# Kernel optimization log

Hardware: AMD Instinct MI355X
Metric: run time of the kernel (lower is better)

Reference implementation:

```python
import jax, jax.numpy as jnp
import numpy as np

B, A, DIN, HID, HEADS, NOUT, K = 256, 64, 64, 128, 4, 2, 7
N = B * A                      # 16384 nodes
C = HID                        # per-head dim == out_channels (module quirk)
SCALE = (HID // HEADS) ** -0.5 # 1/sqrt(32), as in the module


def _xavier(k, shape):
    fan_out, fan_in = shape
    lim = (6.0 / (fan_in + fan_out)) ** 0.5
    return jax.random.uniform(k, shape, jnp.float32, -lim, lim)


def setup_inputs() -> dict:
    key = jax.random.key(0)
    ks = jax.random.split(key, 24)
    x = jax.random.normal(ks[0], (N, DIN), jnp.float32)
    pos_b = jax.random.uniform(ks[1], (B, A, 2), jnp.float32) * 10.0  # [B,A,2]
    pos = pos_b.reshape(N, 2)

    # kNN graph per environment (replicates torch.cdist + topk smallest, drop self)
    d = jnp.linalg.norm(pos_b[:, :, None, :] - pos_b[:, None, :, :], axis=-1)  # [B,A,A]
    _, idx = jax.lax.top_k(-d, K + 1)
    nb = idx[..., 1:]                                   # [B,A,K] neighbor ids
    offs = (jnp.arange(B) * A)[:, None, None]
    src = jnp.broadcast_to(jnp.arange(A)[None, :, None], (B, A, K)) + offs
    dst = nb + offs
    loops = jnp.arange(N)
    edge_index = jnp.stack([
        jnp.concatenate([src.reshape(-1), loops]),
        jnp.concatenate([dst.reshape(-1), loops]),
    ]).astype(jnp.int32)                                # [2, E], E = B*A*K + N

    inp = {"x": x, "pos": pos, "edge_index": edge_index}
    inp["l0_Wq"] = _xavier(ks[2], (HEADS * C, 2))
    inp["l0_Wk"] = _xavier(ks[3], (HEADS * C, 2))
    inp["l0_Wv"] = _xavier(ks[4], (HEADS * C, DIN))
    inp["l0_Wo"] = _xavier(ks[5], (HID, HEADS * C))
    inp["l0_bo"] = jnp.zeros((HID,), jnp.float32)
    inp["l1_Wq"] = _xavier(ks[6], (HEADS * C, 2))
    inp["l1_Wk"] = _xavier(ks[7], (HEADS * C, 2))
    inp["l1_Wv"] = _xavier(ks[8], (HEADS * C, HID))
    inp["l1_Wo"] = _xavier(ks[9], (HID, HEADS * C))
    inp["l1_bo"] = jnp.zeros((HID,), jnp.float32)
    inp["W1"] = _xavier(ks[10], (256, HID))
    inp["b1"] = jnp.zeros((256,), jnp.float32)
    inp["W2"] = _xavier(ks[11], (256, 256))
    inp["b2"] = jnp.zeros((256,), jnp.float32)
    inp["W3"] = _xavier(ks[12], (NOUT, 256))
    inp["b3"] = jnp.zeros((NOUT,), jnp.float32)
    return inp


def _gat(x, pos, src, dst, Wq, Wk, Wv, Wo, bo):
    # positions -> Q/K, features -> V (position-aware attention)
    q = (pos @ Wq.T).reshape(N, HEADS, C)
    k = (pos @ Wk.T).reshape(N, HEADS, C)
    v = (x @ Wv.T).reshape(N, HEADS, C)
    # per-edge logits, segment softmax over incoming edges of dst
    alpha = jnp.einsum('ehc,ehc->eh', q[dst], k[src]) * SCALE        # [E,H]
    amax = jax.ops.segment_max(alpha, dst, num_segments=N)           # [N,H]
    ex = jnp.exp(alpha - amax[dst])
    a = ex / jax.ops.segment_sum(ex, dst, num_segments=N)[dst]
    msg = v[src] * a[..., None]                                      # [E,H,C]
    agg = jax.ops.segment_sum(msg, dst, num_segments=N)              # [N,H,C]
    return agg.reshape(N, HEADS * C) @ Wo.T + bo


def reference(x, pos, edge_index,
              l0_Wq, l0_Wk, l0_Wv, l0_Wo, l0_bo,
              l1_Wq, l1_Wk, l1_Wv, l1_Wo, l1_bo,
              W1, b1, W2, b2, W3, b3):
    src, dst = edge_index[0], edge_index[1]
    h = jnp.tanh(_gat(x, pos, src, dst, l0_Wq, l0_Wk, l0_Wv, l0_Wo, l0_bo))
    h = jnp.tanh(_gat(h, pos, src, dst, l1_Wq, l1_Wk, l1_Wv, l1_Wo, l1_bo))
    h = jax.nn.relu(h @ W1.T + b1)
    h = jax.nn.relu(h @ W2.T + b2)
    out = h @ W3.T + b3
    return out.reshape(B, A, NOUT)
```

## Files before the change

### kernel.cpp

```cpp
#include <hip/hip_runtime.h>
#include <hip/hip_bf16.h>
#include <cstddef>
#include <math.h>

#define N_NODES 16384
#define DIN 64
#define HID 128
#define SCALE_F 0.17677669529663687f

using bf16x8 = __attribute__((ext_vector_type(8))) short;
using f32x4  = __attribute__((ext_vector_type(4))) float;

__device__ __forceinline__ ushort f2b(float x) {
  __hip_bfloat16 h = __float2bfloat16(x);
  return *(ushort*)&h;
}
__device__ __forceinline__ float b2f(ushort u) {
  __hip_bfloat16 h = *(__hip_bfloat16*)&u;
  return __bfloat162float(h);
}
__device__ __forceinline__ void split1(float x, ushort& h, ushort& l) {
  h = f2b(x);
  l = f2b(x - b2f(h));
}
__device__ __forceinline__ void split3(float x, ushort& a, ushort& b, ushort& c) {
  a = f2b(x);
  float r1 = x - b2f(a);
  b = f2b(r1);
  c = f2b(r1 - b2f(b));
}

#define MFMA(d, A, B) d = __builtin_amdgcn_mfma_f32_16x16x32_bf16(A, B, d, 0, 0, 0)


__global__ __launch_bounds__(256) void prep_all_kernel(
    const float* __restrict__ Wq0, const float* __restrict__ Wk0,
    const float* __restrict__ Wq1, const float* __restrict__ Wk1,
    float* __restrict__ G,
    const float* __restrict__ Wv0, const float* __restrict__ Wo0,
    ushort* __restrict__ M0a, ushort* __restrict__ M0b, ushort* __restrict__ M0c,
    const float* __restrict__ Wv1, const float* __restrict__ Wo1,
    ushort* __restrict__ M1a, ushort* __restrict__ M1b, ushort* __restrict__ M1c,
    const float* __restrict__ W1, ushort* __restrict__ W1hi, ushort* __restrict__ W1lo,
    const float* __restrict__ W2, ushort* __restrict__ W2hi, ushort* __restrict__ W2lo,
    unsigned long long* __restrict__ out64)
{
  int blk = blockIdx.x, t = threadIdx.x;
  if (blk == 0) {
    if (t >= 32) return;
    int l = t >> 4, h = (t >> 2) & 3, a = (t >> 1) & 1, b = t & 1;
    const float* Wq = l ? Wq1 : Wq0;
    const float* Wk = l ? Wk1 : Wk0;
    float acc = 0.f;
    for (int c = 0; c < 128; c++)
      acc += Wq[(h * 128 + c) * 2 + a] * Wk[(h * 128 + c) * 2 + b];
    G[t] = acc;
  } else if (blk < 97) {
    int D, gidx;
    const float *Wv, *Wo;
    ushort *Ma, *Mb, *Mc;
    if (blk < 33) { D = DIN; gidx = (blk - 1) * 256 + t;  Wv = Wv0; Wo = Wo0; Ma = M0a; Mb = M0b; Mc = M0c; }
    else          { D = HID; gidx = (blk - 33) * 256 + t; Wv = Wv1; Wo = Wo1; Ma = M1a; Mb = M1b; Mc = M1c; }
    int o = gidx / D, rem = gidx - o * D;
    int qD = D >> 2;
    int h = rem / qD, d0 = (rem - h * qD) * 4;
    const float* wv = Wv + (size_t)(h * 128) * D + d0;
    const float* wo = Wo + (size_t)o * 512 + h * 128;
    float ax = 0.f, ay = 0.f, az = 0.f, aw = 0.f;
    for (int c = 0; c < 128; c++) {
      float4 v = *(const float4*)&wv[(size_t)c * D];
      float w = wo[c];
      ax += v.x * w; ay += v.y * w; az += v.z * w; aw += v.w * w;
    }
    int idx = o * (4 * D) + h * D + d0;
    ushort4 ua, ub, uc;
    split3(ax, ua.x, ub.x, uc.x);
    split3(ay, ua.y, ub.y, uc.y);
    split3(az, ua.z, ub.z, uc.z);
    split3(aw, ua.w, ub.w, uc.w);
    *(ushort4*)&Ma[idx] = ua;
    *(ushort4*)&Mb[idx] = ub;
    *(ushort4*)&Mc[idx] = uc;
  } else if (blk < 193) {
    if (blk < 129) {
      int i = ((blk - 97) * 256 + t) * 4;
      float4 w = *(const float4*)&W1[i];
      ushort4 hi, lo;
      split1(w.x, hi.x, lo.x); split1(w.y, hi.y, lo.y);
      split1(w.z, hi.z, lo.z); split1(w.w, hi.w, lo.w);
      *(ushort4*)&W1hi[i] = hi;
      *(ushort4*)&W1lo[i] = lo;
    } else {
      int j = ((blk - 129) * 256 + t) * 4;
      float4 w = *(const float4*)&W2[j];
      ushort4 hi, lo;
      split1(w.x, hi.x, lo.x); split1(w.y, hi.y, lo.y);
      split1(w.z, hi.z, lo.z); split1(w.w, hi.w, lo.w);
      *(ushort4*)&W2hi[j] = hi;
      *(ushort4*)&W2lo[j] = lo;
    }
  } else {
    int i = (blk - 193) * 256 + t;
    ((float4*)out64)[i] = (float4){0.f, 0.f, 0.f, 0.f};
  }
}


#define SFB_OFF 8192
#define SFC_OFF 16384
#define PXS_OFF 24576
#define PYS_OFF 24704
#define SMASK_OFF 24832
#define AFRAG_OFF 25088
#define PH_OFF 57856
#define LDS_USHORTS 74752

template <int KD>
__device__ __forceinline__ void gat_layer(
    int wave, int lane, int lm, int lq,
    const ushort* sFa, const ushort* sFb, const ushort* sFc,
    ushort* aA,
    const float* pxs, const float* pys,
    const unsigned long long* smask,
    const float* __restrict__ G,
    const ushort* __restrict__ Ma, const ushort* __restrict__ Mb,
    const ushort* __restrict__ Mc,
    f32x4 hacc[4])
{
  constexpr int NKF = KD / 32;
  const int K4 = 4 * KD;
  const int o = 16 * (wave & 7) + lm;
  const int hb = wave >> 3;

  bf16x8 nA, nB, nC;
  {
    size_t boff = (size_t)o * K4 + (2 * hb) * KD + lq * 8;
    nA = *(const bf16x8*)&Ma[boff];
    nB = *(const bf16x8*)&Mb[boff];
    nC = *(const bf16x8*)&Mc[boff];
  }

  {
    int wm = wave & 3;
    int h = wave >> 2;
    float pdxm = pxs[wm * 16 + lm];
    float pdym = pys[wm * 16 + lm];
    unsigned long long mm = smask[wm * 16 + lm];
    unsigned mb0 = (unsigned)((mm >> (8 * lq)) & 0xFF);
    unsigned mb1 = (unsigned)((mm >> (32 + 8 * lq)) & 0xFF);
    float g0 = G[h * 4], g1 = G[h * 4 + 1], g2 = G[h * 4 + 2], g3 = G[h * 4 + 3];
    float a0 = (g0 * pdxm + g2 * pdym) * SCALE_F;
    float a1 = (g1 * pdxm + g3 * pdym) * SCALE_F;
    float sshift = a0 * pdxm + a1 * pdym;
    float e[16];
    float sum = 0.f;
#pragma unroll
    for (int j = 0; j < 8; j++) {
      e[j]     = ((mb0 >> j) & 1) ? __expf(a0 * pxs[8 * lq + j] + a1 * pys[8 * lq + j] - sshift) : 0.f;
      e[8 + j] = ((mb1 >> j) & 1) ? __expf(a0 * pxs[32 + 8 * lq + j] + a1 * pys[32 + 8 * lq + j] - sshift) : 0.f;
      sum += e[j] + e[8 + j];
    }
    sum += __shfl_xor(sum, 16);
    sum += __shfl_xor(sum, 32);
    float inv = 1.f / sum;
    bf16x8 Aa0, Aa1, Ab0, Ab1;
#pragma unroll
    for (int j = 0; j < 8; j++) {
      ushort ua, ub;
      split1(e[j] * inv, ua, ub);     Aa0[j] = (short)ua; Ab0[j] = (short)ub;
      split1(e[8 + j] * inv, ua, ub); Aa1[j] = (short)ua; Ab1[j] = (short)ub;
    }
    int sbase = wave * 2048 + lane * 8;
    *(bf16x8*)&aA[sbase]        = Aa0;
    *(bf16x8*)&aA[sbase + 512]  = Aa1;
    *(bf16x8*)&aA[sbase + 1024] = Ab0;
    *(bf16x8*)&aA[sbase + 1536] = Ab1;
  }
  __syncthreads();

#pragma unroll
  for (int i = 0; i < 4; i++) hacc[i] = (f32x4){0.f, 0.f, 0.f, 0.f};

#pragma unroll 1
  for (int hi = 0; hi < 2; hi++) {
    int h = 2 * hb + hi;
    f32x4 y[4];
#pragma unroll
    for (int i = 0; i < 4; i++) y[i] = (f32x4){0.f, 0.f, 0.f, 0.f};
#pragma unroll 1
    for (int kf = 0; kf < NKF; kf++) {
      int ko = kf * 32 + lq * 8;
      int sw = lm << 3;
      bf16x8 ma = nA, mb = nB, mc = nC;
#pragma unroll
      for (int mp = 0; mp < 2; mp++) {
        int f0 = (mp * 32 + lm) * 128 + (ko ^ sw);
        int f1 = f0 + 16 * 128;
        bf16x8 fa0 = *(const bf16x8*)&sFa[f0], fa1 = *(const bf16x8*)&sFa[f1];
        bf16x8 fb0 = *(const bf16x8*)&sFb[f0], fb1 = *(const bf16x8*)&sFb[f1];
        bf16x8 fc0 = *(const bf16x8*)&sFc[f0], fc1 = *(const bf16x8*)&sFc[f1];
        f32x4 y0 = y[mp * 2], y1 = y[mp * 2 + 1];
        MFMA(y0, fa0, ma); MFMA(y1, fa1, ma);
        MFMA(y0, fa0, mb); MFMA(y1, fa1, mb);
        MFMA(y0, fb0, ma); MFMA(y1, fb1, ma);
        MFMA(y0, fa0, mc); MFMA(y1, fa1, mc);
        MFMA(y0, fc0, ma); MFMA(y1, fc1, ma);
        MFMA(y0, fb0, mb); MFMA(y1, fb1, mb);
        y[mp * 2] = y0; y[mp * 2 + 1] = y1;
      }
      if (hi == 0 || kf != NKF - 1) {
        int hn = (kf == NKF - 1) ? (h + 1) : h;
        int kn = (kf == NKF - 1) ? 0 : (kf + 1);
        size_t boff = (size_t)o * K4 + hn * KD + kn * 32 + lq * 8;
        nA = *(const bf16x8*)&Ma[boff];
        nB = *(const bf16x8*)&Mb[boff];
        nC = *(const bf16x8*)&Mc[boff];
      }
    }
    bf16x8 Ya[2], Yb[2];
#pragma unroll
    for (int kb = 0; kb < 2; kb++) {
#pragma unroll
      for (int j = 0; j < 8; j++) {
        int sl = ((2 * lq + (j >> 2)) & 3) * 16 + lm;
        float v0 = __shfl(y[2 * kb][j & 3], sl);
        float v1 = __shfl(y[2 * kb + 1][j & 3], sl);
        float v = (lq & 2) ? v1 : v0;
        ushort ua, ub;
        split1(v, ua, ub);
        Ya[kb][j] = (short)ua; Yb[kb][j] = (short)ub;
      }
    }
#pragma unroll
    for (int mtd = 0; mtd < 4; mtd++) {
      int abase = (h * 4 + mtd) * 2048 + lane * 8;
      bf16x8 Aa0 = *(const bf16x8*)&aA[abase];
      bf16x8 Aa1 = *(const bf16x8*)&aA[abase + 512];
      bf16x8 Ab0 = *(const bf16x8*)&aA[abase + 1024];
      bf16x8 Ab1 = *(const bf16x8*)&aA[abase + 1536];
      MFMA(hacc[mtd], Aa0, Ya[0]);
      MFMA(hacc[mtd], Aa0, Yb[0]);
      MFMA(hacc[mtd], Ab0, Ya[0]);
      MFMA(hacc[mtd], Ab0, Yb[0]);
      MFMA(hacc[mtd], Aa1, Ya[1]);
      MFMA(hacc[mtd], Aa1, Yb[1]);
      MFMA(hacc[mtd], Ab1, Ya[1]);
      MFMA(hacc[mtd], Ab1, Yb[1]);
    }
  }
}

__global__ __attribute__((amdgpu_flat_work_group_size(1024, 1024), amdgpu_waves_per_eu(4, 4)))
void fused_gat_kernel(
    const float* __restrict__ x, const float* __restrict__ pos,
    const int* __restrict__ srcp, const int* __restrict__ dstp,
    const float* __restrict__ G,
    const ushort* __restrict__ M0a, const ushort* __restrict__ M0b, const ushort* __restrict__ M0c,
    const ushort* __restrict__ M1a, const ushort* __restrict__ M1b, const ushort* __restrict__ M1c,
    const float* __restrict__ bo0, const float* __restrict__ bo1,
    const ushort* __restrict__ W1hi, const ushort* __restrict__ W1lo, const float* __restrict__ b1,
    const ushort* __restrict__ W2hi, const ushort* __restrict__ W2lo, const float* __restrict__ b2,
    const float* __restrict__ W3, const float* __restrict__ b3,
    float* __restrict__ outp)
{
  __shared__ __align__(16) ushort uBig[LDS_USHORTS];
  ushort* sFa = uBig;
  ushort* sFb = uBig + SFB_OFF;
  ushort* sFc = uBig + SFC_OFF;
  float* pxs = (float*)(uBig + PXS_OFF);
  float* pys = (float*)(uBig + PYS_OFF);
  unsigned long long* smask = (unsigned long long*)(uBig + SMASK_OFF);
  ushort* aA = uBig + AFRAG_OFF;
  ushort* pA = uBig + AFRAG_OFF;
  ushort* pB = uBig + AFRAG_OFF + 16384;
  float* pH = (float*)(uBig + PH_OFF);

  int b = blockIdx.x, t = threadIdx.x;
  int wave = t >> 6, lane = t & 63, lm = lane & 15, lq = lane >> 4;
  int o = 16 * (wave & 7) + lm;

  int e_s = 0, e_d = 0;
  if (t < 448) {
    e_s = srcp[b * 448 + t];
    e_d = dstp[b * 448 + t];
  }
  float posx = 0.f, posy = 0.f;
  if (t < 64) {
    posx = pos[(b * 64 + t) * 2];
    posy = pos[(b * 64 + t) * 2 + 1];
  }
  const float4* gx = (const float4*)(x + (size_t)b * 64 * DIN);
  float4 xv = gx[t];
  float bv0 = bo0[o];
  float bv1 = bo1[o];

  if (t < 64) {
    pxs[t] = posx;
    pys[t] = posy;
    smask[t] = 1ull << t;
  }
  {
    int r = t >> 4, c = (t & 15) * 4;
    int cs = c ^ ((r & 15) << 3);
    ushort4 ua, ub, uc;
    split3(xv.x, ua.x, ub.x, uc.x); split3(xv.y, ua.y, ub.y, uc.y);
    split3(xv.z, ua.z, ub.z, uc.z); split3(xv.w, ua.w, ub.w, uc.w);
    *(ushort4*)&sFa[r * 128 + cs] = ua;
    *(ushort4*)&sFb[r * 128 + cs] = ub;
    *(ushort4*)&sFc[r * 128 + cs] = uc;
  }
  __syncthreads();
  if (t < 448) {
    atomicOr(&smask[e_d & 63], 1ull << (e_s & 63));
  }
  __syncthreads();

  f32x4 hacc[4];
  gat_layer<DIN>(wave, lane, lm, lq, sFa, sFb, sFc, aA, pxs, pys, smask,
                 G, M0a, M0b, M0c, hacc);
  if (wave >= 8) {
#pragma unroll
    for (int mtd = 0; mtd < 4; mtd++)
#pragma unroll
      for (int r = 0; r < 4; r++)
        pH[(mtd * 16 + lq * 4 + r) * 132 + o] = hacc[mtd][r];
  }
  __syncthreads();
  if (wave < 8) {
#pragma unroll
    for (int mtd = 0; mtd < 4; mtd++)
#pragma unroll
      for (int r = 0; r < 4; r++) {
        int dst = mtd * 16 + lq * 4 + r;
        float v = tanhf(hacc[mtd][r] + pH[dst * 132 + o] + bv0);
        ushort ua, ub, uc;
        split3(v, ua, ub, uc);
        int cs = o ^ ((dst & 15) << 3);
        sFa[dst * 128 + cs] = ua;
        sFb[dst * 128 + cs] = ub;
        sFc[dst * 128 + cs] = uc;
      }
  }
  __syncthreads();
  gat_layer<HID>(wave, lane, lm, lq, sFa, sFb, sFc, aA, pxs, pys, smask,
                 G + 16, M1a, M1b, M1c, hacc);

  int col = 16 * wave + lm;
  bf16x8 pw1h[4], pw1l[4];
#pragma unroll
  for (int kf = 0; kf < 4; kf++) {
    int ko = kf * 32 + lq * 8;
    pw1h[kf] = *(const bf16x8*)&W1hi[(size_t)col * 128 + ko];
    pw1l[kf] = *(const bf16x8*)&W1lo[(size_t)col * 128 + ko];
  }
  float b1v = b1[col];

  if (wave >= 8) {
#pragma unroll
    for (int mtd = 0; mtd < 4; mtd++)
#pragma unroll
      for (int r = 0; r < 4; r++)
        pH[(mtd * 16 + lq * 4 + r) * 132 + o] = hacc[mtd][r];
  }
  __syncthreads();
  if (wave < 8) {
#pragma unroll
    for (int mtd = 0; mtd < 4; mtd++)
#pragma unroll
      for (int r = 0; r < 4; r++) {
        int dst = mtd * 16 + lq * 4 + r;
        float v = tanhf(hacc[mtd][r] + pH[dst * 132 + o] + bv1);
        ushort hh, ll;
        split1(v, hh, ll);
        int cs = o ^ ((dst & 15) << 3);
        sFa[dst * 128 + cs] = hh;
        sFb[dst * 128 + cs] = ll;
      }
  }
  __syncthreads();
  f32x4 y1[4];
#pragma unroll
  for (int mtd = 0; mtd < 4; mtd++) y1[mtd] = (f32x4){0.f, 0.f, 0.f, 0.f};
#pragma unroll
  for (int kf = 0; kf < 4; kf++) {
    int ko = kf * 32 + lq * 8;
    bf16x8 bh = pw1h[kf];
    bf16x8 bl = pw1l[kf];
#pragma unroll
    for (int mtd = 0; mtd < 4; mtd++) {
      int row = mtd * 16 + lm;
      int cs = ko ^ (lm << 3);
      bf16x8 ah = *(const bf16x8*)&sFa[row * 128 + cs];
      bf16x8 al = *(const bf16x8*)&sFb[row * 128 + cs];
      MFMA(y1[mtd], ah, bh);
      MFMA(y1[mtd], ah, bl);
      MFMA(y1[mtd], al, bh);
    }
  }
  {
#pragma unroll
    for (int mtd = 0; mtd < 4; mtd++)
#pragma unroll
      for (int r = 0; r < 4; r++) {
        int row = mtd * 16 + lq * 4 + r;
        float v = fmaxf(y1[mtd][r] + b1v, 0.f);
        ushort hh, ll;
        split1(v, hh, ll);
        int cc = col ^ ((row & 15) << 3);
        pA[row * 256 + cc] = hh;
        pB[row * 256 + cc] = ll;
      }
  }
  bf16x8 pw2h[8], pw2l[8];
#pragma unroll
  for (int kf = 0; kf < 8; kf++) {
    int ko = kf * 32 + lq * 8;
    pw2h[kf] = *(const bf16x8*)&W2hi[(size_t)col * 256 + ko];
    pw2l[kf] = *(const bf16x8*)&W2lo[(size_t)col * 256 + ko];
  }
  float w30 = W3[col], w31 = W3[256 + col];
  float b20 = b2[col];
  float bb0 = (wave == 0) ? b3[0] : 0.f;
  float bb1 = (wave == 0) ? b3[1] : 0.f;
  __syncthreads();
  f32x4 y2[4];
#pragma unroll
  for (int mtd = 0; mtd < 4; mtd++) y2[mtd] = (f32x4){0.f, 0.f, 0.f, 0.f};
#pragma unroll
  for (int kf = 0; kf < 8; kf++) {
    int ko = kf * 32 + lq * 8;
    bf16x8 bh = pw2h[kf];
    bf16x8 bl = pw2l[kf];
#pragma unroll
    for (int mtd = 0; mtd < 4; mtd++) {
      int row = mtd * 16 + lm;
      int cc = ko ^ (lm << 3);
      bf16x8 ah = *(const bf16x8*)&pA[row * 256 + cc];
      bf16x8 al = *(const bf16x8*)&pB[row * 256 + cc];
      MFMA(y2[mtd], ah, bh);
      MFMA(y2[mtd], ah, bl);
      MFMA(y2[mtd], al, bh);
    }
  }
  {
#pragma unroll
    for (int mtd = 0; mtd < 4; mtd++)
#pragma unroll
      for (int r = 0; r < 4; r++) {
        float va = fmaxf(y2[mtd][r] + b20, 0.f);
        float s0 = va * w30;
        float s1 = va * w31;
        s0 += __shfl_xor(s0, 1); s0 += __shfl_xor(s0, 2);
        s0 += __shfl_xor(s0, 4); s0 += __shfl_xor(s0, 8);
        s1 += __shfl_xor(s1, 1); s1 += __shfl_xor(s1, 2);
        s1 += __shfl_xor(s1, 4); s1 += __shfl_xor(s1, 8);
        if (lm == 0) {
          int row = b * 64 + mtd * 16 + lq * 4 + r;
          atomicAdd(&outp[row * 2 + 0], s0 + bb0);
          atomicAdd(&outp[row * 2 + 1], s1 + bb1);
        }
      }
  }
}


extern "C" void kernel_launch(void* const* d_in, const int* in_sizes, int n_in,
                              void* d_out, int out_size, void* d_ws, size_t ws_size,
                              hipStream_t stream) {
  const float* x     = (const float*)d_in[0];
  const float* pos   = (const float*)d_in[1];
  const int*   ei    = (const int*)d_in[2];
  const float* l0_Wq = (const float*)d_in[3];
  const float* l0_Wk = (const float*)d_in[4];
  const float* l0_Wv = (const float*)d_in[5];
  const float* l0_Wo = (const float*)d_in[6];
  const float* l0_bo = (const float*)d_in[7];
  const float* l1_Wq = (const float*)d_in[8];
  const float* l1_Wk = (const float*)d_in[9];
  const float* l1_Wv = (const float*)d_in[10];
  const float* l1_Wo = (const float*)d_in[11];
  const float* l1_bo = (const float*)d_in[12];
  const float* W1    = (const float*)d_in[13];
  const float* b1    = (const float*)d_in[14];
  const float* W2    = (const float*)d_in[15];
  const float* b2    = (const float*)d_in[16];
  const float* W3    = (const float*)d_in[17];
  const float* b3    = (const float*)d_in[18];
  float* outp = (float*)d_out;

  int E = in_sizes[2] / 2;
  const int* srcp = ei;
  const int* dstp = ei + E;

  char* base = (char*)d_ws;
  size_t off = 0;
  auto alloc = [&](size_t bytes) -> void* {
    void* p = base + off;
    off = (off + bytes + 255) & ~(size_t)255;
    return p;
  };
  float*  G   = (float*)alloc(32 * sizeof(float));
  ushort* M0a = (ushort*)alloc((size_t)128 * 256 * 2);
  ushort* M0b = (ushort*)alloc((size_t)128 * 256 * 2);
  ushort* M0c = (ushort*)alloc((size_t)128 * 256 * 2);
  ushort* M1a = (ushort*)alloc((size_t)128 * 512 * 2);
  ushort* M1b = (ushort*)alloc((size_t)128 * 512 * 2);
  ushort* M1c = (ushort*)alloc((size_t)128 * 512 * 2);
  ushort* W1hi = (ushort*)alloc((size_t)256 * 128 * 2);
  ushort* W1lo = (ushort*)alloc((size_t)256 * 128 * 2);
  ushort* W2hi = (ushort*)alloc((size_t)256 * 256 * 2);
  ushort* W2lo = (ushort*)alloc((size_t)256 * 256 * 2);

  prep_all_kernel<<<225, 256, 0, stream>>>(
      l0_Wq, l0_Wk, l1_Wq, l1_Wk, G,
      l0_Wv, l0_Wo, M0a, M0b, M0c,
      l1_Wv, l1_Wo, M1a, M1b, M1c,
      W1, W1hi, W1lo, W2, W2hi, W2lo,
      (unsigned long long*)outp);

  fused_gat_kernel<<<N_NODES / 64, 1024, 0, stream>>>(
      x, pos, srcp, dstp, G, M0a, M0b, M0c, M1a, M1b, M1c, l0_bo, l1_bo,
      W1hi, W1lo, b1, W2hi, W2lo, b2, W3, b3, outp);

  (void)n_in; (void)out_size; (void)ws_size;
}
```

Baseline: 155.0 us.

## Overlap layer-1 attention build with tanh epilogue and prefetch weight fragments

Attention-coefficient construction is split out into build_A. For layer 1 it now runs on waves 8-15 while waves 0-7 do the layer-0 tanh/split epilogue, and each of those idle waves builds two pair slots. This removes one __syncthreads and the serial softmax phase before the second GAT layer. Weight fragments for both layers are also loaded earlier, before the preceding work, to hide global latency, at the cost of more live registers. It assumes the aA region does not alias the pH or sF buffers written during that phase.

```diff
diff --git a/kernel.cpp b/kernel.cpp
--- a/kernel.cpp
+++ b/kernel.cpp
@@ -115,7 +115,48 @@
 #define PH_OFF 57856
 #define LDS_USHORTS 74752
 
-template <int KD>
+__device__ __forceinline__ void build_A(
+    int pairid, int lane, int lm, int lq, ushort* aA,
+    const float* pxs, const float* pys,
+    const unsigned long long* smask, const float* __restrict__ G)
+{
+  int wm = pairid & 3;
+  int h = pairid >> 2;
+  float pdxm = pxs[wm * 16 + lm];
+  float pdym = pys[wm * 16 + lm];
+  unsigned long long mm = smask[wm * 16 + lm];
+  unsigned mb0 = (unsigned)((mm >> (8 * lq)) & 0xFF);
+  unsigned mb1 = (unsigned)((mm >> (32 + 8 * lq)) & 0xFF);
+  float g0 = G[h * 4], g1 = G[h * 4 + 1], g2 = G[h * 4 + 2], g3 = G[h * 4 + 3];
+  float a0 = (g0 * pdxm + g2 * pdym) * SCALE_F;
+  float a1 = (g1 * pdxm + g3 * pdym) * SCALE_F;
+  float sshift = a0 * pdxm + a1 * pdym;
+  float e[16];
+  float sum = 0.f;
+#pragma unroll
+  for (int j = 0; j < 8; j++) {
+    e[j]     = ((mb0 >> j) & 1) ? __expf(a0 * pxs[8 * lq + j] + a1 * pys[8 * lq + j] - sshift) : 0.f;
+    e[8 + j] = ((mb1 >> j) & 1) ? __expf(a0 * pxs[32 + 8 * lq + j] + a1 * pys[32 + 8 * lq + j] - sshift) : 0.f;
+    sum += e[j] + e[8 + j];
+  }
+  sum += __shfl_xor(sum, 16);
+  sum += __shfl_xor(sum, 32);
+  float inv = 1.f / sum;
+  bf16x8 Aa0, Aa1, Ab0, Ab1;
+#pragma unroll
+  for (int j = 0; j < 8; j++) {
+    ushort ua, ub;
+    split1(e[j] * inv, ua, ub);     Aa0[j] = (short)ua; Ab0[j] = (short)ub;
+    split1(e[8 + j] * inv, ua, ub); Aa1[j] = (short)ua; Ab1[j] = (short)ub;
+  }
+  int sbase = pairid * 2048 + lane * 8;
+  *(bf16x8*)&aA[sbase]        = Aa0;
+  *(bf16x8*)&aA[sbase + 512]  = Aa1;
+  *(bf16x8*)&aA[sbase + 1024] = Ab0;
+  *(bf16x8*)&aA[sbase + 1536] = Ab1;
+}
+
+template <int KD, bool BUILD_A>
 __device__ __forceinline__ void gat_layer(
     int wave, int lane, int lm, int lq,
     const ushort* sFa, const ushort* sFb, const ushort* sFc,
@@ -125,6 +166,7 @@
     const float* __restrict__ G,
     const ushort* __restrict__ Ma, const ushort* __restrict__ Mb,
     const ushort* __restrict__ Mc,
+    bf16x8 nA, bf16x8 nB, bf16x8 nC,
     f32x4 hacc[4])
 {
   constexpr int NKF = KD / 32;
@@ -132,51 +174,10 @@
   const int o = 16 * (wave & 7) + lm;
   const int hb = wave >> 3;
 
-  bf16x8 nA, nB, nC;
-  {
-    size_t boff = (size_t)o * K4 + (2 * hb) * KD + lq * 8;
-    nA = *(const bf16x8*)&Ma[boff];
-    nB = *(const bf16x8*)&Mb[boff];
-    nC = *(const bf16x8*)&Mc[boff];
-  }
-
-  {
-    int wm = wave & 3;
-    int h = wave >> 2;
-    float pdxm = pxs[wm * 16 + lm];
-    float pdym = pys[wm * 16 + lm];
-    unsigned long long mm = smask[wm * 16 + lm];
-    unsigned mb0 = (unsigned)((mm >> (8 * lq)) & 0xFF);
-    unsigned mb1 = (unsigned)((mm >> (32 + 8 * lq)) & 0xFF);
-    float g0 = G[h * 4], g1 = G[h * 4 + 1], g2 = G[h * 4 + 2], g3 = G[h * 4 + 3];
-    float a0 = (g0 * pdxm + g2 * pdym) * SCALE_F;
-    float a1 = (g1 * pdxm + g3 * pdym) * SCALE_F;
-    float sshift = a0 * pdxm + a1 * pdym;
-    float e[16];
-    float sum = 0.f;
-#pragma unroll
-    for (int j = 0; j < 8; j++) {
-      e[j]     = ((mb0 >> j) & 1) ? __expf(a0 * pxs[8 * lq + j] + a1 * pys[8 * lq + j] - sshift) : 0.f;
-      e[8 + j] = ((mb1 >> j) & 1) ? __expf(a0 * pxs[32 + 8 * lq + j] + a1 * pys[32 + 8 * lq + j] - sshift) : 0.f;
-      sum += e[j] + e[8 + j];
-    }
-    sum += __shfl_xor(sum, 16);
-    sum += __shfl_xor(sum, 32);
-    float inv = 1.f / sum;
-    bf16x8 Aa0, Aa1, Ab0, Ab1;
-#pragma unroll
-    for (int j = 0; j < 8; j++) {
-      ushort ua, ub;
-      split1(e[j] * inv, ua, ub);     Aa0[j] = (short)ua; Ab0[j] = (short)ub;
-      split1(e[8 + j] * inv, ua, ub); Aa1[j] = (short)ua; Ab1[j] = (short)ub;
-    }
-    int sbase = wave * 2048 + lane * 8;
-    *(bf16x8*)&aA[sbase]        = Aa0;
-    *(bf16x8*)&aA[sbase + 512]  = Aa1;
-    *(bf16x8*)&aA[sbase + 1024] = Ab0;
-    *(bf16x8*)&aA[sbase + 1536] = Ab1;
-  }
-  __syncthreads();
+  if (BUILD_A) {
+    build_A(wave, lane, lm, lq, aA, pxs, pys, smask, G);
+    __syncthreads();
+  }
 
 #pragma unroll
   for (int i = 0; i < 4; i++) hacc[i] = (f32x4){0.f, 0.f, 0.f, 0.f};
@@ -293,6 +294,13 @@
   float4 xv = gx[t];
   float bv0 = bo0[o];
   float bv1 = bo1[o];
+  bf16x8 m0A, m0B, m0C;
+  {
+    size_t boff = (size_t)o * (4 * DIN) + ((wave >> 3) * 2) * DIN + lq * 8;
+    m0A = *(const bf16x8*)&M0a[boff];
+    m0B = *(const bf16x8*)&M0b[boff];
+    m0C = *(const bf16x8*)&M0c[boff];
+  }
 
   if (t < 64) {
     pxs[t] = posx;
@@ -316,8 +324,17 @@
   __syncthreads();
 
   f32x4 hacc[4];
-  gat_layer<DIN>(wave, lane, lm, lq, sFa, sFb, sFc, aA, pxs, pys, smask,
-                 G, M0a, M0b, M0c, hacc);
+  gat_layer<DIN, true>(wave, lane, lm, lq, sFa, sFb, sFc, aA, pxs, pys, smask,
+                       G, M0a, M0b, M0c, m0A, m0B, m0C, hacc);
+
+  bf16x8 m1A, m1B, m1C;
+  {
+    size_t boff = (size_t)o * (4 * HID) + ((wave >> 3) * 2) * HID + lq * 8;
+    m1A = *(const bf16x8*)&M1a[boff];
+    m1B = *(const bf16x8*)&M1b[boff];
+    m1C = *(const bf16x8*)&M1c[boff];
+  }
+
   if (wave >= 8) {
 #pragma unroll
     for (int mtd = 0; mtd < 4; mtd++)
@@ -340,10 +357,13 @@
         sFb[dst * 128 + cs] = ub;
         sFc[dst * 128 + cs] = uc;
       }
-  }
-  __syncthreads();
-  gat_layer<HID>(wave, lane, lm, lq, sFa, sFb, sFc, aA, pxs, pys, smask,
-                 G + 16, M1a, M1b, M1c, hacc);
+  } else {
+    build_A(wave - 8, lane, lm, lq, aA, pxs, pys, smask, G + 16);
+    build_A(wave,     lane, lm, lq, aA, pxs, pys, smask, G + 16);
+  }
+  __syncthreads();
+  gat_layer<HID, false>(wave, lane, lm, lq, sFa, sFb, sFc, aA, pxs, pys, smask,
+                        G + 16, M1a, M1b, M1c, m1A, m1B, m1C, hacc);
 
   int col = 16 * wave + lm;
   bf16x8 pw1h[4], pw1l[4];
```

Result: no change. 153.3 us (-1.1%).
